# Optimization experiments

Hardware: AMD Instinct MI355X
Metric: run time of the kernel (lower is better)

## Reference

```python
import jax, jax.numpy as jnp
import numpy as np
import math

ALPHAS = [0.5, 1.0]
LSTM_SIZE = 512
LSTM_LAYERS = 2
OUTPUT_SIZE = 1024
INPUT_SIZE = 250


def _inv_gamma(z):
    # 1/gamma(z); gamma has poles at non-positive integers -> 1/gamma = 0 (matches scipy: gamma(0)=inf)
    if z <= 0 and float(z) == int(z):
        return 0.0
    return 1.0 / math.gamma(z)


def _caputo(x, alpha):
    # x: (B, T, N). D[t] = coef * sum_{j<t} (x[t]-x[j]) * (t-j+1e-6)^(-alpha)
    T = x.shape[1]
    t = jnp.arange(T, dtype=jnp.float32)
    diff = t[:, None] - t[None, :]
    W = jnp.where(diff > 0, (jnp.abs(diff) + 1e-6) ** (-alpha), 0.0)  # (T, T) strictly lower triangular
    coef = _inv_gamma(1.0 - alpha)
    rowsum = W.sum(axis=1)  # (T,)
    # coef * (x[t] * sum_j W[t,j] - sum_j W[t,j] x[j])
    return coef * (x * rowsum[None, :, None] - jnp.einsum('tj,bjn->btn', W, x))


def _lstm_layer(x, Wih, Whh, bih, bhh):
    # x: (B, T, F); torch LSTM gate order i, f, g, o
    B = x.shape[0]
    H = Whh.shape[1]
    xW = jnp.einsum('btf,gf->btg', x, Wih) + bih + bhh  # (B, T, 4H)
    h0 = jnp.zeros((B, H), dtype=x.dtype)
    c0 = jnp.zeros((B, H), dtype=x.dtype)

    def step(carry, xt):
        h, c = carry
        gates = xt + h @ Whh.T
        i, f, g, o = jnp.split(gates, 4, axis=-1)
        i = jax.nn.sigmoid(i)
        f = jax.nn.sigmoid(f)
        g = jnp.tanh(g)
        o = jax.nn.sigmoid(o)
        c = f * c + i * g
        h = o * jnp.tanh(c)
        return (h, c), h

    _, hs = jax.lax.scan(step, (h0, c0), jnp.swapaxes(xW, 0, 1))  # hs: (T, B, H)
    return jnp.swapaxes(hs, 0, 1)


def setup_inputs() -> dict:
    key = jax.random.key(0)
    ks = jax.random.split(key, 12)
    B, T, N = 64, 512, INPUT_SIZE
    H = LSTM_SIZE
    F_in = N * len(ALPHAS)
    s0 = 1.0 / math.sqrt(H)
    inp = {
        'x': jax.random.normal(ks[0], (B, T, N), dtype=jnp.float32),
        'Wih0': jax.random.uniform(ks[1], (4 * H, F_in), minval=-s0, maxval=s0, dtype=jnp.float32),
        'Whh0': jax.random.uniform(ks[2], (4 * H, H), minval=-s0, maxval=s0, dtype=jnp.float32),
        'bih0': jax.random.uniform(ks[3], (4 * H,), minval=-s0, maxval=s0, dtype=jnp.float32),
        'bhh0': jax.random.uniform(ks[4], (4 * H,), minval=-s0, maxval=s0, dtype=jnp.float32),
        'Wih1': jax.random.uniform(ks[5], (4 * H, H), minval=-s0, maxval=s0, dtype=jnp.float32),
        'Whh1': jax.random.uniform(ks[6], (4 * H, H), minval=-s0, maxval=s0, dtype=jnp.float32),
        'bih1': jax.random.uniform(ks[7], (4 * H,), minval=-s0, maxval=s0, dtype=jnp.float32),
        'bhh1': jax.random.uniform(ks[8], (4 * H,), minval=-s0, maxval=s0, dtype=jnp.float32),
        'Wout': jax.random.uniform(ks[9], (OUTPUT_SIZE, H), minval=-s0, maxval=s0, dtype=jnp.float32),
        'bout': jax.random.uniform(ks[10], (OUTPUT_SIZE,), minval=-s0, maxval=s0, dtype=jnp.float32),
    }
    return inp


def reference(x, Wih0, Whh0, bih0, bhh0, Wih1, Whh1, bih1, bhh1, Wout, bout):
    feats = jnp.concatenate([_caputo(x, a) for a in ALPHAS], axis=2)  # (B, T, N*len(alphas))
    h = _lstm_layer(feats, Wih0, Whh0, bih0, bhh0)
    h = _lstm_layer(h, Wih1, Whh1, bih1, bhh1)
    last = h[:, -1, :]
    return jax.nn.relu(last @ Wout.T + bout)
```

## Files before the change

### kernel.cpp

```cpp
#include <hip/hip_runtime.h>
#include <cstddef>

#define BB 64
#define TT 512
#define NN 250
#define HH 512
#define NB (NN*BB)
#define HB (HH*BB)
#define K0 762
#define K1 1024

#define AGENT __HIP_MEMORY_SCOPE_AGENT

__device__ __forceinline__ float sigmoidf_(float x) { return 1.0f / (1.0f + expf(-x)); }

__device__ __forceinline__ float coh_ld(const float* p) {
    return __hip_atomic_load(p, __ATOMIC_RELAXED, AGENT);
}
__device__ __forceinline__ void coh_st(float* p, float v) {
    __hip_atomic_store(p, v, __ATOMIC_RELAXED, AGENT);
}

__global__ __launch_bounds__(256) void k_transpose(const float* __restrict__ x,
                                                   float* __restrict__ xT) {
    const int t = blockIdx.x;
    const int n = blockIdx.y * 4 + (threadIdx.x >> 6);
    const int b = threadIdx.x & 63;
    if (n < NN)
        xT[(size_t)t * NB + n * BB + b] = x[(size_t)b * (TT * NN) + t * NN + n];
}

__global__ __launch_bounds__(512) void k_wrow(float* __restrict__ w, float* __restrict__ rowsum) {
    __shared__ float sw[TT];
    const int d = threadIdx.x;
    const float wd = (d >= 1) ? (1.0f / sqrtf((float)d + 1e-6f)) : 0.0f;
    sw[d] = wd;
    w[d] = wd;
    __syncthreads();
    float s = 0.0f;
    for (int j = 1; j <= d; ++j) s += sw[j];
    rowsum[d] = s;
}

__global__ __launch_bounds__(256) void k_caputo(const float* __restrict__ xT,
                                                const float* __restrict__ w,
                                                const float* __restrict__ rowsum,
                                                float* __restrict__ featsT) {
    const float COEF = 0.5641895835477563f;
    const int t0 = blockIdx.x * 4;
    const int nb0 = blockIdx.y * 1024 + threadIdx.x;
    float acc[4][4];
#pragma unroll
    for (int a = 0; a < 4; ++a)
#pragma unroll
        for (int e = 0; e < 4; ++e) acc[a][e] = 0.0f;

    for (int j = 0; j < t0; ++j) {
        const float* xj = xT + (size_t)j * NB;
        const float wt0 = w[t0 - j];
        const float wt1 = w[t0 + 1 - j];
        const float wt2 = w[t0 + 2 - j];
        const float wt3 = w[t0 + 3 - j];
#pragma unroll
        for (int e = 0; e < 4; ++e) {
            const int nb = nb0 + e * 256;
            const float xv = (nb < NB) ? xj[nb] : 0.0f;
            acc[0][e] = fmaf(wt0, xv, acc[0][e]);
            acc[1][e] = fmaf(wt1, xv, acc[1][e]);
            acc[2][e] = fmaf(wt2, xv, acc[2][e]);
            acc[3][e] = fmaf(wt3, xv, acc[3][e]);
        }
    }
#pragma unroll
    for (int dj = 0; dj < 3; ++dj) {
        const int j = t0 + dj;
        const float* xj = xT + (size_t)j * NB;
#pragma unroll
        for (int e = 0; e < 4; ++e) {
            const int nb = nb0 + e * 256;
            const float xv = (nb < NB) ? xj[nb] : 0.0f;
#pragma unroll
            for (int tt = 0; tt < 4; ++tt)
                if (tt > dj) acc[tt][e] = fmaf(w[tt - dj], xv, acc[tt][e]);
        }
    }
#pragma unroll
    for (int tt = 0; tt < 4; ++tt) {
        const int t = t0 + tt;
        const float rs = rowsum[t];
        const float* xt = xT + (size_t)t * NB;
        float* ft = featsT + (size_t)t * NB;
#pragma unroll
        for (int e = 0; e < 4; ++e) {
            const int nb = nb0 + e * 256;
            if (nb < NB) ft[nb] = COEF * fmaf(xt[nb], rs, -acc[tt][e]);
        }
    }
}

__global__ __launch_bounds__(256) void k_wt(const float* __restrict__ Wih0,
                                            const float* __restrict__ Whh0,
                                            const float* __restrict__ Wih1,
                                            const float* __restrict__ Whh1,
                                            float* __restrict__ WT0b,
                                            float* __restrict__ WT1b) {
    const int total0 = 128 * K0 * 16;
    const int total1 = 128 * K1 * 16;
    const int stride = gridDim.x * 256;
    for (int idx = blockIdx.x * 256 + threadIdx.x; idx < total0; idx += stride) {
        const int r = idx & 15;
        const int k = (idx >> 4) % K0;
        const int bi = idx / (16 * K0);
        const int row = (r & 3) * HH + bi * 4 + (r >> 2);
        WT0b[idx] = (k < NN) ? Wih0[(size_t)row * 500 + k] : Whh0[(size_t)row * HH + (k - NN)];
    }
    for (int idx = blockIdx.x * 256 + threadIdx.x; idx < total1; idx += stride) {
        const int r = idx & 15;
        const int k = (idx >> 4) % K1;
        const int bi = idx / (16 * K1);
        const int row = (r & 3) * HH + bi * 4 + (r >> 2);
        WT1b[idx] = (k < HH) ? Wih1[(size_t)row * HH + k] : Whh1[(size_t)row * HH + (k - HH)];
    }
}

__device__ __forceinline__ void gridbar(unsigned* leaf, unsigned* ggen,
                                        unsigned* root, unsigned* gen,
                                        unsigned target, int tid) {
    __syncthreads();
    if (tid == 0) {
        if (__hip_atomic_fetch_add(leaf, 1u, __ATOMIC_RELAXED, AGENT) == 7u) {
            __hip_atomic_store(leaf, 0u, __ATOMIC_RELAXED, AGENT);
            if (__hip_atomic_fetch_add(root, 1u, __ATOMIC_RELAXED, AGENT) == 31u) {
                __hip_atomic_store(root, 0u, __ATOMIC_RELAXED, AGENT);
                __hip_atomic_fetch_add(gen, 1u, __ATOMIC_RELAXED, AGENT);
            } else {
                while (__hip_atomic_load(gen, __ATOMIC_RELAXED, AGENT) < target)
                    __builtin_amdgcn_s_sleep(1);
            }
            __hip_atomic_fetch_add(ggen, 1u, __ATOMIC_RELAXED, AGENT);
        } else {
            while (__hip_atomic_load(ggen, __ATOMIC_RELAXED, AGENT) < target)
                __builtin_amdgcn_s_sleep(1);
        }
    }
    __syncthreads();
}

__global__ __launch_bounds__(1024, 4) void k_persist(
    const float* __restrict__ featsT,
    const float* __restrict__ WT0b, const float* __restrict__ WT1b,
    const float* __restrict__ bih0, const float* __restrict__ bhh0,
    const float* __restrict__ bih1, const float* __restrict__ bhh1,
    float* __restrict__ h0T, float* __restrict__ h1T,
    unsigned* __restrict__ bar) {
    __shared__ float wlds[16384];
    __shared__ float part[16384];
    const int tid = threadIdx.x;
    const int b = tid & 63;
    const int wv = tid >> 6;
    const int bid = blockIdx.x;
    const bool isL1 = (bid >= 128);
    const int bi = isL1 ? (bid - 128) : bid;

    unsigned* leaf = bar + (bid >> 3) * 32;
    unsigned* ggen = bar + 1024 + (bid >> 3) * 32;
    unsigned* root = bar + 2048;
    unsigned* gen  = bar + 2080;

    {
        const float* __restrict__ wsrc = isL1 ? (WT1b + (size_t)bi * (K1 * 16))
                                              : (WT0b + (size_t)bi * (K0 * 16));
        const int nflt = (isL1 ? K1 : K0) * 16;
        for (int i = tid * 4; i < nflt; i += 4096)
            *reinterpret_cast<float4*>(&wlds[i]) = *reinterpret_cast<const float4*>(wsrc + i);
    }
    float bsum[4] = {0.f, 0.f, 0.f, 0.f};
    float creg = 0.0f;
    if (wv < 4) {
        const int hu = bi * 4 + wv;
        const float* __restrict__ bi_ = isL1 ? bih1 : bih0;
        const float* __restrict__ bh_ = isL1 ? bhh1 : bhh0;
#pragma unroll
        for (int g = 0; g < 4; ++g) bsum[g] = bi_[g * HH + hu] + bh_[g * HH + hu];
    }
    __syncthreads();

#define FMA16(KIDX, VV)                                                         \
    {                                                                           \
        const float4* wl = reinterpret_cast<const float4*>(&wlds[(KIDX) * 16]); \
        const float4 w0_ = wl[0], w1_ = wl[1], w2_ = wl[2], w3_ = wl[3];        \
        acc[0] = fmaf(w0_.x, (VV), acc[0]);   acc[1] = fmaf(w0_.y, (VV), acc[1]);  \
        acc[2] = fmaf(w0_.z, (VV), acc[2]);   acc[3] = fmaf(w0_.w, (VV), acc[3]);  \
        acc[4] = fmaf(w1_.x, (VV), acc[4]);   acc[5] = fmaf(w1_.y, (VV), acc[5]);  \
        acc[6] = fmaf(w1_.z, (VV), acc[6]);   acc[7] = fmaf(w1_.w, (VV), acc[7]);  \
        acc[8] = fmaf(w2_.x, (VV), acc[8]);   acc[9] = fmaf(w2_.y, (VV), acc[9]);  \
        acc[10] = fmaf(w2_.z, (VV), acc[10]); acc[11] = fmaf(w2_.w, (VV), acc[11]); \
        acc[12] = fmaf(w3_.x, (VV), acc[12]); acc[13] = fmaf(w3_.y, (VV), acc[13]); \
        acc[14] = fmaf(w3_.z, (VV), acc[14]); acc[15] = fmaf(w3_.w, (VV), acc[15]); \
    }

    for (int s = 0; s <= TT; ++s) {
        const bool active = isL1 ? (s >= 1) : (s < TT);
        if (active) {
            const int rd = (s + 1) & 1;
            const float* __restrict__ h0rd = h0T + (size_t)rd * HB;
            float acc[16];
#pragma unroll
            for (int r = 0; r < 16; ++r) acc[r] = 0.0f;

            if (!isL1) {
                const int k0 = wv * 48;
                int k1 = k0 + 48; if (k1 > K0) k1 = K0;
                {
                    const float* __restrict__ vf = featsT + (size_t)s * NB + b;
                    const int e = (k1 < NN) ? k1 : NN;
                    int k = k0;
                    for (; k + 8 <= e; k += 8) {
                        float v[8];
#pragma unroll
                        for (int j = 0; j < 8; ++j) v[j] = vf[(size_t)(k + j) * 64];
#pragma unroll
                        for (int j = 0; j < 8; ++j) FMA16(k + j, v[j])
                    }
                    for (; k < e; ++k) { const float vv = vf[(size_t)k * 64]; FMA16(k, vv) }
                }
                {
                    const float* __restrict__ vh = h0rd + b;
                    const int st = (k0 > NN) ? k0 : NN;
                    int k = st;
                    for (; k + 8 <= k1; k += 8) {
                        float v[8];
#pragma unroll
                        for (int j = 0; j < 8; ++j) v[j] = coh_ld(&vh[(size_t)(k - NN + j) * 64]);
#pragma unroll
                        for (int j = 0; j < 8; ++j) FMA16(k + j, v[j])
                    }
                    for (; k < k1; ++k) { const float vv = coh_ld(&vh[(size_t)(k - NN) * 64]); FMA16(k, vv) }
                }
            } else {
                const int k0 = wv * 64;
                const float* __restrict__ vbase =
                    (k0 < HH) ? (h0rd + b) : (h1T + (size_t)rd * HB + b);
                const int koff = (k0 < HH) ? k0 : (k0 - HH);
#pragma unroll 1
                for (int c = 0; c < 64; c += 8) {
                    float v[8];
#pragma unroll
                    for (int j = 0; j < 8; ++j) v[j] = coh_ld(&vbase[(size_t)(koff + c + j) * 64]);
#pragma unroll
                    for (int j = 0; j < 8; ++j) FMA16(k0 + c + j, v[j])
                }
            }

#pragma unroll
            for (int r = 0; r < 16; ++r) part[(wv * 16 + r) * 64 + b] = acc[r];
            __syncthreads();

            if (wv < 4) {
                float g4[4];
#pragma unroll
                for (int g = 0; g < 4; ++g) {
                    float sum = bsum[g];
#pragma unroll
                    for (int i = 0; i < 16; ++i) sum += part[(i * 16 + wv * 4 + g) * 64 + b];
                    g4[g] = sum;
                }
                const float gi = sigmoidf_(g4[0]);
                const float gf = sigmoidf_(g4[1]);
                const float gg = tanhf(g4[2]);
                const float go = sigmoidf_(g4[3]);
                const float cn = fmaf(gf, creg, gi * gg);
                creg = cn;
                const int hu = bi * 4 + wv;
                float* __restrict__ hT = (isL1 ? h1T : h0T) + (size_t)(s & 1) * HB;
                coh_st(&hT[hu * 64 + b], go * tanhf(cn));
            }
        }
        gridbar(leaf, ggen, root, gen, (unsigned)(s + 1), tid);
    }
#undef FMA16
}

__global__ __launch_bounds__(256) void k_out(const float* __restrict__ h1T,
                                             const float* __restrict__ Wout,
                                             const float* __restrict__ bout,
                                             float* __restrict__ out) {
    const int o = blockIdx.x * 4 + (threadIdx.x >> 6);
    const int b = threadIdx.x & 63;
    float acc = 0.0f;
    const float* wrow = Wout + (size_t)o * HH;
    for (int k = 0; k < HH; k += 4) {
        const float4 wv = *reinterpret_cast<const float4*>(wrow + k);
        acc = fmaf(wv.x, h1T[(k + 0) * BB + b],
              fmaf(wv.y, h1T[(k + 1) * BB + b],
              fmaf(wv.z, h1T[(k + 2) * BB + b],
              fmaf(wv.w, h1T[(k + 3) * BB + b], acc))));
    }
    acc += bout[o];
    out[(size_t)b * 1024 + o] = fmaxf(acc, 0.0f);
}

extern "C" void kernel_launch(void* const* d_in, const int* in_sizes, int n_in,
                              void* d_out, int out_size, void* d_ws, size_t ws_size,
                              hipStream_t stream) {
    (void)in_sizes; (void)n_in; (void)out_size; (void)ws_size;
    const float* x    = (const float*)d_in[0];
    const float* Wih0 = (const float*)d_in[1];
    const float* Whh0 = (const float*)d_in[2];
    const float* bih0 = (const float*)d_in[3];
    const float* bhh0 = (const float*)d_in[4];
    const float* Wih1 = (const float*)d_in[5];
    const float* Whh1 = (const float*)d_in[6];
    const float* bih1 = (const float*)d_in[7];
    const float* bhh1 = (const float*)d_in[8];
    const float* Wout = (const float*)d_in[9];
    const float* bout = (const float*)d_in[10];

    float* ws     = (float*)d_ws;
    float* xT     = ws;
    float* WT0b   = ws;
    float* WT1b   = WT0b + (size_t)128 * K0 * 16;
    float* featsT = xT + (size_t)TT * NB;
    float* w      = featsT + (size_t)TT * NB;
    float* rowsum = w + TT;
    float* h0T    = rowsum + TT;
    float* h1T    = h0T + 2 * (size_t)HB;
    unsigned* bar = (unsigned*)(h1T + 2 * (size_t)HB);

    hipMemsetAsync(h0T, 0, (size_t)4 * HB * sizeof(float), stream);
    hipMemsetAsync(bar, 0, 4096 * sizeof(unsigned), stream);

    k_transpose<<<dim3(TT, 63), 256, 0, stream>>>(x, xT);
    k_wrow<<<1, TT, 0, stream>>>(w, rowsum);
    k_caputo<<<dim3(TT / 4, 16), 256, 0, stream>>>(xT, w, rowsum, featsT);
    k_wt<<<512, 256, 0, stream>>>(Wih0, Whh0, Wih1, Whh1, WT0b, WT1b);

    void* args[] = {(void*)&featsT, (void*)&WT0b, (void*)&WT1b,
                    (void*)&bih0, (void*)&bhh0, (void*)&bih1, (void*)&bhh1,
                    (void*)&h0T, (void*)&h1T, (void*)&bar};
    hipLaunchCooperativeKernel((void*)k_persist, dim3(256), dim3(1024), args, 0, stream);

    k_out<<<256, 256, 0, stream>>>(h1T, Wout, bout, (float*)d_out);
}
```

Baseline: 6.577 ms.

## Simplify grid barrier, double-buffer vector loads, use fast gate activations

```diff
diff --git a/kernel.cpp b/kernel.cpp
--- a/kernel.cpp
+++ b/kernel.cpp
@@ -12,7 +12,8 @@
 
 #define AGENT __HIP_MEMORY_SCOPE_AGENT
 
-__device__ __forceinline__ float sigmoidf_(float x) { return 1.0f / (1.0f + expf(-x)); }
+__device__ __forceinline__ float fsig(float x)  { return 1.0f / (1.0f + __expf(-x)); }
+__device__ __forceinline__ float ftanh(float x) { return 1.0f - 2.0f / (__expf(2.0f * x) + 1.0f); }
 
 __device__ __forceinline__ float coh_ld(const float* p) {
     return __hip_atomic_load(p, __ATOMIC_RELAXED, AGENT);
@@ -123,8 +124,7 @@
     }
 }
 
-__device__ __forceinline__ void gridbar(unsigned* leaf, unsigned* ggen,
-                                        unsigned* root, unsigned* gen,
+__device__ __forceinline__ void gridbar(unsigned* leaf, unsigned* root, unsigned* gen,
                                         unsigned target, int tid) {
     __syncthreads();
     if (tid == 0) {
@@ -132,18 +132,74 @@
             __hip_atomic_store(leaf, 0u, __ATOMIC_RELAXED, AGENT);
             if (__hip_atomic_fetch_add(root, 1u, __ATOMIC_RELAXED, AGENT) == 31u) {
                 __hip_atomic_store(root, 0u, __ATOMIC_RELAXED, AGENT);
-                __hip_atomic_fetch_add(gen, 1u, __ATOMIC_RELAXED, AGENT);
-            } else {
-                while (__hip_atomic_load(gen, __ATOMIC_RELAXED, AGENT) < target)
-                    __builtin_amdgcn_s_sleep(1);
+                __hip_atomic_store(gen, target, __ATOMIC_RELAXED, AGENT);
             }
-            __hip_atomic_fetch_add(ggen, 1u, __ATOMIC_RELAXED, AGENT);
+        }
+        while (__hip_atomic_load(gen, __ATOMIC_RELAXED, AGENT) < target) {}
+    }
+    __syncthreads();
+}
+
+__device__ __forceinline__ void fma16(const float* __restrict__ wlds, int k, float vv,
+                                      float* __restrict__ acc) {
+    const float4* wl = reinterpret_cast<const float4*>(wlds + (size_t)k * 16);
+    const float4 w0 = wl[0], w1 = wl[1], w2 = wl[2], w3 = wl[3];
+    acc[0]  = fmaf(w0.x, vv, acc[0]);   acc[1]  = fmaf(w0.y, vv, acc[1]);
+    acc[2]  = fmaf(w0.z, vv, acc[2]);   acc[3]  = fmaf(w0.w, vv, acc[3]);
+    acc[4]  = fmaf(w1.x, vv, acc[4]);   acc[5]  = fmaf(w1.y, vv, acc[5]);
+    acc[6]  = fmaf(w1.z, vv, acc[6]);   acc[7]  = fmaf(w1.w, vv, acc[7]);
+    acc[8]  = fmaf(w2.x, vv, acc[8]);   acc[9]  = fmaf(w2.y, vv, acc[9]);
+    acc[10] = fmaf(w2.z, vv, acc[10]);  acc[11] = fmaf(w2.w, vv, acc[11]);
+    acc[12] = fmaf(w3.x, vv, acc[12]);  acc[13] = fmaf(w3.y, vv, acc[13]);
+    acc[14] = fmaf(w3.z, vv, acc[14]);  acc[15] = fmaf(w3.w, vv, acc[15]);
+}
+
+template<bool COH>
+__device__ __forceinline__ float ldv(const float* p) {
+    if constexpr (COH) return coh_ld(p);
+    else return *p;
+}
+
+template<bool COH>
+__device__ __forceinline__ void dot_seg(const float* __restrict__ vsrc, int kb, int ke,
+                                        const float* __restrict__ wlds,
+                                        float* __restrict__ acc) {
+    int k = kb;
+    const int n8 = (ke - k) >> 3;
+    float va[8], vb[8];
+    if (n8 > 0) {
+#pragma unroll
+        for (int j = 0; j < 8; ++j) va[j] = ldv<COH>(vsrc + (size_t)(k + j) * 64);
+        int c = 0;
+        while (c + 2 < n8) {
+#pragma unroll
+            for (int j = 0; j < 8; ++j) vb[j] = ldv<COH>(vsrc + (size_t)(k + 8 + j) * 64);
+#pragma unroll
+            for (int j = 0; j < 8; ++j) fma16(wlds, k + j, va[j], acc);
+            k += 8;
+#pragma unroll
+            for (int j = 0; j < 8; ++j) va[j] = ldv<COH>(vsrc + (size_t)(k + 8 + j) * 64);
+#pragma unroll
+            for (int j = 0; j < 8; ++j) fma16(wlds, k + j, vb[j], acc);
+            k += 8;
+            c += 2;
+        }
+        if (c + 2 == n8) {
+#pragma unroll
+            for (int j = 0; j < 8; ++j) vb[j] = ldv<COH>(vsrc + (size_t)(k + 8 + j) * 64);
+#pragma unroll
+            for (int j = 0; j < 8; ++j) fma16(wlds, k + j, va[j], acc);
+            k += 8;
+#pragma unroll
+            for (int j = 0; j < 8; ++j) fma16(wlds, k + j, vb[j], acc);
+            k += 8;
         } else {
-            while (__hip_atomic_load(ggen, __ATOMIC_RELAXED, AGENT) < target)
-                __builtin_amdgcn_s_sleep(1);
-        }
-    }
-    __syncthreads();
+#pragma unroll
+            for (int j = 0; j < 8; ++j) fma16(wlds, k + j, va[j], acc);
+            k += 8;
+        }
+    }
+    for (; k < ke; ++k) fma16(wlds, k, ldv<COH>(vsrc + (size_t)k * 64), acc);
 }
 
 __global__ __launch_bounds__(1024, 4) void k_persist(
@@ -163,7 +219,6 @@
     const int bi = isL1 ? (bid - 128) : bid;
 
     unsigned* leaf = bar + (bid >> 3) * 32;
-    unsigned* ggen = bar + 1024 + (bid >> 3) * 32;
     unsigned* root = bar + 2048;
     unsigned* gen  = bar + 2080;
 
@@ -185,20 +240,6 @@
     }
     __syncthreads();
 
-#define FMA16(KIDX, VV)                                                         \
-    {                                                                           \
-        const float4* wl = reinterpret_cast<const float4*>(&wlds[(KIDX) * 16]); \
-        const float4 w0_ = wl[0], w1_ = wl[1], w2_ = wl[2], w3_ = wl[3];        \
-        acc[0] = fmaf(w0_.x, (VV), acc[0]);   acc[1] = fmaf(w0_.y, (VV), acc[1]);  \
-        acc[2] = fmaf(w0_.z, (VV), acc[2]);   acc[3] = fmaf(w0_.w, (VV), acc[3]);  \
-        acc[4] = fmaf(w1_.x, (VV), acc[4]);   acc[5] = fmaf(w1_.y, (VV), acc[5]);  \
-        acc[6] = fmaf(w1_.z, (VV), acc[6]);   acc[7] = fmaf(w1_.w, (VV), acc[7]);  \
-        acc[8] = fmaf(w2_.x, (VV), acc[8]);   acc[9] = fmaf(w2_.y, (VV), acc[9]);  \
-        acc[10] = fmaf(w2_.z, (VV), acc[10]); acc[11] = fmaf(w2_.w, (VV), acc[11]); \
-        acc[12] = fmaf(w3_.x, (VV), acc[12]); acc[13] = fmaf(w3_.y, (VV), acc[13]); \
-        acc[14] = fmaf(w3_.z, (VV), acc[14]); acc[15] = fmaf(w3_.w, (VV), acc[15]); \
-    }
-
     for (int s = 0; s <= TT; ++s) {
         const bool active = isL1 ? (s >= 1) : (s < TT);
         if (active) {
@@ -214,42 +255,19 @@
                 {
                     const float* __restrict__ vf = featsT + (size_t)s * NB + b;
                     const int e = (k1 < NN) ? k1 : NN;
-                    int k = k0;
-                    for (; k + 8 <= e; k += 8) {
-                        float v[8];
-#pragma unroll
-                        for (int j = 0; j < 8; ++j) v[j] = vf[(size_t)(k + j) * 64];
-#pragma unroll
-                        for (int j = 0; j < 8; ++j) FMA16(k + j, v[j])
-                    }
-                    for (; k < e; ++k) { const float vv = vf[(size_t)k * 64]; FMA16(k, vv) }
+                    if (k0 < e) dot_seg<false>(vf, k0, e, wlds, acc);
                 }
                 {
-                    const float* __restrict__ vh = h0rd + b;
+                    const float* __restrict__ vh = h0rd + (ptrdiff_t)b - (ptrdiff_t)NN * 64;
                     const int st = (k0 > NN) ? k0 : NN;
-                    int k = st;
-                    for (; k + 8 <= k1; k += 8) {
-                        float v[8];
-#pragma unroll
-                        for (int j = 0; j < 8; ++j) v[j] = coh_ld(&vh[(size_t)(k - NN + j) * 64]);
-#pragma unroll
-                        for (int j = 0; j < 8; ++j) FMA16(k + j, v[j])
-                    }
-                    for (; k < k1; ++k) { const float vv = coh_ld(&vh[(size_t)(k - NN) * 64]); FMA16(k, vv) }
+                    if (st < k1) dot_seg<true>(vh, st, k1, wlds, acc);
                 }
             } else {
                 const int k0 = wv * 64;
-                const float* __restrict__ vbase =
-                    (k0 < HH) ? (h0rd + b) : (h1T + (size_t)rd * HB + b);
-                const int koff = (k0 < HH) ? k0 : (k0 - HH);
-#pragma unroll 1
-                for (int c = 0; c < 64; c += 8) {
-                    float v[8];
-#pragma unroll
-                    for (int j = 0; j < 8; ++j) v[j] = coh_ld(&vbase[(size_t)(koff + c + j) * 64]);
-#pragma unroll
-                    for (int j = 0; j < 8; ++j) FMA16(k0 + c + j, v[j])
-                }
+                const float* __restrict__ vb =
+                    (k0 < HH) ? (h0rd + b)
+                              : (h1T + (size_t)rd * HB + (ptrdiff_t)b - (ptrdiff_t)HH * 64);
+                dot_seg<true>(vb, k0, k0 + 64, wlds, acc);
             }
 
 #pragma unroll
@@ -265,20 +283,19 @@
                     for (int i = 0; i < 16; ++i) sum += part[(i * 16 + wv * 4 + g) * 64 + b];
                     g4[g] = sum;
                 }
-                const float gi = sigmoidf_(g4[0]);
-                const float gf = sigmoidf_(g4[1]);
-                const float gg = tanhf(g4[2]);
-                const float go = sigmoidf_(g4[3]);
+                const float gi = fsig(g4[0]);
+                const float gf = fsig(g4[1]);
+                const float gg = ftanh(g4[2]);
+                const float go = fsig(g4[3]);
                 const float cn = fmaf(gf, creg, gi * gg);
                 creg = cn;
                 const int hu = bi * 4 + wv;
                 float* __restrict__ hT = (isL1 ? h1T : h0T) + (size_t)(s & 1) * HB;
-                coh_st(&hT[hu * 64 + b], go * tanhf(cn));
+                coh_st(&hT[hu * 64 + b], go * ftanh(cn));
             }
         }
-        gridbar(leaf, ggen, root, gen, (unsigned)(s + 1), tid);
-    }
-#undef FMA16
+        gridbar(leaf, root, gen, (unsigned)(s + 1), tid);
+    }
 }
 
 __global__ __launch_bounds__(256) void k_out(const float* __restrict__ h1T,
```

New measurement: 14.48 ms. 120% more time.
